# Optimization experiments

Measured on AMD Instinct MI355X. Metric: run time of the kernel, lower is better.

## Reference

```python
import jax, jax.numpy as jnp
import numpy as np

N_ATOMS = 4096
N_NEIGH = 32
IN_F = 128
HID = 256
OUT_F = 128
N_SPECIES = 64


def setup_inputs() -> dict:
    key = jax.random.key(0)
    k1, k2, k3, k4, k5, k6 = jax.random.split(key, 6)
    # kaiming-uniform-ish init scales (exact init doesn't matter for correctness testing)
    s1 = 1.0 / np.sqrt(IN_F)
    s2 = 1.0 / np.sqrt(HID)
    return {
        "features": jax.random.normal(k1, (N_ATOMS, N_NEIGH, IN_F), dtype=jnp.float32),
        "species_idx": jax.random.randint(k2, (N_ATOMS,), 0, N_SPECIES, dtype=jnp.int64 if jax.config.jax_enable_x64 else jnp.int32),
        "W1": jax.random.uniform(k3, (N_SPECIES, HID, IN_F), jnp.float32, -s1, s1),
        "b1": jax.random.uniform(k4, (N_SPECIES, HID), jnp.float32, -s1, s1),
        "W2": jax.random.uniform(k5, (N_SPECIES, OUT_F, HID), jnp.float32, -s2, s2),
        "b2": jax.random.uniform(k6, (N_SPECIES, OUT_F), jnp.float32, -s2, s2),
    }


def reference(features, species_idx, W1, b1, W2, b2):
    # Per-atom species-conditioned 2-layer MLP with SiLU after the hidden layer.
    # features: (A, N, in); W[idx]: (A, out, in) gathered per atom (as in torch W[idx]).
    x = jnp.einsum("ani,ahi->anh", features, W1[species_idx]) + b1[species_idx][:, None, :]
    x = jax.nn.silu(x)
    x = jnp.einsum("anh,aoh->ano", x, W2[species_idx]) + b2[species_idx][:, None, :]
    return x  # (A, N, out)
```

## Files before the change

kernel.cpp:

```cpp
#include <hip/hip_runtime.h>

typedef __attribute__((ext_vector_type(8))) short short8;
typedef __attribute__((ext_vector_type(4))) float f32x4;

#define N_ATOMS 4096
#define N_NEIGH 32
#define IN_F 128
#define HID 256
#define OUT_F 128
#define N_SPECIES 64
#define GRP 4
#define MAX_GROUPS 1088

struct HL { short h, l; };
__device__ __forceinline__ HL split2(float v) {
  unsigned u = __float_as_uint(v);
  float lo = v - __uint_as_float(u & 0xFFFF0000u);
  HL o;
  o.h = (short)(u >> 16);
  o.l = (short)(__float_as_uint(lo) >> 16);
  return o;
}

__global__ __launch_bounds__(256) void prep_kernel(
    const float* __restrict__ W1, const float* __restrict__ W2,
    const int* __restrict__ sp_idx,
    unsigned short* __restrict__ w1h, unsigned short* __restrict__ w1l,
    unsigned short* __restrict__ w2h, unsigned short* __restrict__ w2l,
    int* __restrict__ atom_order, int* __restrict__ grp_sp,
    int* __restrict__ grp_base, int* __restrict__ grp_cnt,
    int* __restrict__ n_groups) {
  const int t = threadIdx.x;
  if (blockIdx.x == 0) {
    __shared__ int cnt[N_SPECIES], off[N_SPECIES], cur[N_SPECIES], gb[N_SPECIES];
    if (t < N_SPECIES) cnt[t] = 0;
    __syncthreads();
    for (int a = t; a < N_ATOMS; a += 256) atomicAdd(&cnt[sp_idx[a]], 1);
    __syncthreads();
    if (t == 0) {
      int o = 0, g = 0;
      for (int s = 0; s < N_SPECIES; ++s) {
        off[s] = o; cur[s] = o; gb[s] = g;
        o += cnt[s];
        g += (cnt[s] + GRP - 1) / GRP;
      }
      *n_groups = g;
    }
    __syncthreads();
    for (int a = t; a < N_ATOMS; a += 256) {
      int s = sp_idx[a];
      atom_order[atomicAdd(&cur[s], 1)] = a;
    }
    if (t < N_SPECIES) {
      const int c = cnt[t], base = off[t], g0 = gb[t];
      const int ng = (c + GRP - 1) / GRP;
      for (int j = 0; j < ng; ++j) {
        grp_sp[g0 + j]   = t;
        grp_base[g0 + j] = base + j * GRP;
        grp_cnt[g0 + j]  = min(GRP, c - j * GRP);
      }
    }
    return;
  }
  const int NV = (N_SPECIES * HID * IN_F) / 4;
  const int nsplit = (gridDim.x - 1) * 256;
  for (int v = (blockIdx.x - 1) * 256 + t; v < 2 * NV; v += nsplit) {
    const float4* src; unsigned short* dh; unsigned short* dl; int j;
    if (v < NV) { src = (const float4*)W1; dh = w1h; dl = w1l; j = v; }
    else        { src = (const float4*)W2; dh = w2h; dl = w2l; j = v - NV; }
    float4 f = src[j];
    float vv[4] = {f.x, f.y, f.z, f.w};
    ushort4 h, l;
    HL s0 = split2(vv[0]); h.x = (unsigned short)s0.h; l.x = (unsigned short)s0.l;
    HL s1 = split2(vv[1]); h.y = (unsigned short)s1.h; l.y = (unsigned short)s1.l;
    HL s2 = split2(vv[2]); h.z = (unsigned short)s2.h; l.z = (unsigned short)s2.l;
    HL s3 = split2(vv[3]); h.w = (unsigned short)s3.h; l.w = (unsigned short)s3.l;
    ((ushort4*)dh)[j] = h;
    ((ushort4*)dl)[j] = l;
  }
}

__global__ __launch_bounds__(256, 2) void mlp_kernel(
    const float* __restrict__ feat,
    const float* __restrict__ b1g, const float* __restrict__ b2g,
    const unsigned short* __restrict__ w1h, const unsigned short* __restrict__ w1l,
    const unsigned short* __restrict__ w2h, const unsigned short* __restrict__ w2l,
    const int* __restrict__ atom_order, const int* __restrict__ grp_sp,
    const int* __restrict__ grp_base, const int* __restrict__ grp_cnt,
    const int* __restrict__ n_groups,
    float* __restrict__ out) {
  const int g = blockIdx.x;
  if (g >= *n_groups) return;
  const int s = grp_sp[g];
  const int abase = grp_base[g];
  const int cnt = grp_cnt[g];
  const int tid = threadIdx.x;
  const int wave = tid >> 6, lane = tid & 63;
  const int q = lane >> 4, r = lane & 15;

  __shared__ short8 lw1[2][2][512];
  __shared__ short8 lw2[2][2][512];
  __shared__ float lx[4][N_NEIGH * 32];

  const bool active = (wave < cnt);
  int atom = 0;

  int srcoff[8];
  const char* gplane;
  int hcstride;
  if (wave < 2) {
    gplane = (const char*)(wave == 0 ? w1h : w1l) + (long)s * (HID * IN_F) * 2;
    hcstride = 32 * IN_F * 2;
#pragma unroll
    for (int it = 0; it < 8; ++it) {
      const int d = it * 64 + lane;
      const int ks = d >> 7, ht = (d >> 6) & 1, rr = (d >> 2) & 15, qq = d & 3;
      srcoff[it] = (16 * ht + rr) * (IN_F * 2) + (32 * ks + 8 * qq) * 2;
    }
  } else {
    gplane = (const char*)(wave == 2 ? w2h : w2l) + (long)s * (OUT_F * HID) * 2;
    hcstride = 32 * 2;
#pragma unroll
    for (int it = 0; it < 8; ++it) {
      const int d = it * 64 + lane;
      const int ot = d >> 6, rr = (d >> 2) & 15, qq = d & 3;
      srcoff[it] = (16 * ot + rr) * (HID * 2) + qq * 16;
    }
  }
  short8* dst0 = (wave < 2) ? &lw1[0][wave][0] : &lw2[0][wave - 2][0];

  auto STAGE = [&](int buf, int hc) {
    const char* base = gplane + hc * hcstride;
    short8* dst = dst0 + buf * 1024;
#pragma unroll
    for (int it = 0; it < 8; ++it) {
      __builtin_amdgcn_global_load_lds(
          (const __attribute__((address_space(1))) unsigned int*)(base + srcoff[it]),
          (__attribute__((address_space(3))) unsigned int*)(dst + it * 64 + lane),
          16, 0, 0);
    }
  };

  STAGE(0, 0);

  short8 fh[2][4], fl[2][4];
  if (active) {
    atom = atom_order[abase + wave];
    const float* fb = feat + (long)atom * (N_NEIGH * IN_F);
#pragma unroll
    for (int nt = 0; nt < 2; ++nt)
#pragma unroll
      for (int ks = 0; ks < 4; ++ks) {
        const float* p = fb + (16 * nt + r) * IN_F + 32 * ks + 8 * q;
        float4 v0 = *(const float4*)p;
        float4 v1 = *(const float4*)(p + 4);
        float vv[8] = {v0.x, v0.y, v0.z, v0.w, v1.x, v1.y, v1.z, v1.w};
        short8 h8, l8;
#pragma unroll
        for (int j = 0; j < 8; ++j) {
          HL hl = split2(vv[j]);
          h8[j] = hl.h;
          l8[j] = hl.l;
        }
        fh[nt][ks] = h8;
        fl[nt][ks] = l8;
      }
  }

  float b2v[8];
#pragma unroll
  for (int ot = 0; ot < 8; ++ot) b2v[ot] = b2g[s * OUT_F + 16 * ot + r];

  f32x4 oacc[2][8] = {};
  char* lxw = (char*)lx[wave];
  const int slotbase = r * 4 + q;

  asm volatile("s_waitcnt vmcnt(0)" ::: "memory");
  __syncthreads();

  for (int hc = 0; hc < 8; ++hc) {
    const int buf = hc & 1;
    if (hc < 7) STAGE(buf ^ 1, hc + 1);

    if (active) {
      f32x4 xacc[2][2] = {};
#pragma unroll
      for (int ks = 0; ks < 4; ++ks)
#pragma unroll
        for (int ht = 0; ht < 2; ++ht) {
          short8 bh = lw1[buf][0][(ks * 2 + ht) * 64 + slotbase];
          short8 bl = lw1[buf][1][(ks * 2 + ht) * 64 + slotbase];
#pragma unroll
          for (int nt = 0; nt < 2; ++nt) {
            xacc[nt][ht] = __builtin_amdgcn_mfma_f32_16x16x32_bf16(fh[nt][ks], bh, xacc[nt][ht], 0, 0, 0);
            xacc[nt][ht] = __builtin_amdgcn_mfma_f32_16x16x32_bf16(fh[nt][ks], bl, xacc[nt][ht], 0, 0, 0);
            xacc[nt][ht] = __builtin_amdgcn_mfma_f32_16x16x32_bf16(fl[nt][ks], bh, xacc[nt][ht], 0, 0, 0);
          }
        }
#pragma unroll
      for (int ht = 0; ht < 2; ++ht) {
        const float b1v = b1g[s * HID + hc * 32 + 16 * ht + r];
#pragma unroll
        for (int nt = 0; nt < 2; ++nt)
#pragma unroll
          for (int i = 0; i < 4; ++i) {
            const int n = 16 * nt + 4 * q + i;
            float v = xacc[nt][ht][i] + b1v;
            v = v * __builtin_amdgcn_rcpf(1.0f + __expf(-v));
            int byte = (n << 7) + ((r + 16 * ht) << 2);
            byte ^= (n & 7) << 4;
            *(float*)(lxw + byte) = v;
          }
      }
      short8 ah[2], al[2];
#pragma unroll
      for (int nt = 0; nt < 2; ++nt) {
        const int n = 16 * nt + r;
        const int base_b = (n << 7) + (q << 5);
        const int swz = (n & 7) << 4;
        float4 v0 = *(const float4*)(lxw + (base_b ^ swz));
        float4 v1 = *(const float4*)(lxw + ((base_b + 16) ^ swz));
        float vv[8] = {v0.x, v0.y, v0.z, v0.w, v1.x, v1.y, v1.z, v1.w};
        short8 h8, l8;
#pragma unroll
        for (int j = 0; j < 8; ++j) {
          HL hl = split2(vv[j]);
          h8[j] = hl.h;
          l8[j] = hl.l;
        }
        ah[nt] = h8;
        al[nt] = l8;
      }
#pragma unroll
      for (int ot = 0; ot < 8; ++ot) {
        short8 bh = lw2[buf][0][ot * 64 + slotbase];
        short8 bl = lw2[buf][1][ot * 64 + slotbase];
#pragma unroll
        for (int nt = 0; nt < 2; ++nt) {
          oacc[nt][ot] = __builtin_amdgcn_mfma_f32_16x16x32_bf16(ah[nt], bh, oacc[nt][ot], 0, 0, 0);
          oacc[nt][ot] = __builtin_amdgcn_mfma_f32_16x16x32_bf16(ah[nt], bl, oacc[nt][ot], 0, 0, 0);
          oacc[nt][ot] = __builtin_amdgcn_mfma_f32_16x16x32_bf16(al[nt], bh, oacc[nt][ot], 0, 0, 0);
        }
      }
    }
    asm volatile("s_waitcnt vmcnt(0)" ::: "memory");
    __syncthreads();
  }

  if (active) {
    float* ob = out + (long)atom * (N_NEIGH * OUT_F);
#pragma unroll
    for (int nt = 0; nt < 2; ++nt)
#pragma unroll
      for (int ot = 0; ot < 8; ++ot)
#pragma unroll
        for (int i = 0; i < 4; ++i) {
          ob[(16 * nt + 4 * q + i) * OUT_F + 16 * ot + r] = oacc[nt][ot][i] + b2v[ot];
        }
  }
}

extern "C" void kernel_launch(void* const* d_in, const int* in_sizes, int n_in,
                              void* d_out, int out_size, void* d_ws, size_t ws_size,
                              hipStream_t stream) {
  const float* feat = (const float*)d_in[0];
  const int* sp     = (const int*)d_in[1];
  const float* W1   = (const float*)d_in[2];
  const float* b1   = (const float*)d_in[3];
  const float* W2   = (const float*)d_in[4];
  const float* b2   = (const float*)d_in[5];
  float* out = (float*)d_out;

  char* ws = (char*)d_ws;
  unsigned short* w1h = (unsigned short*)(ws + 0);
  unsigned short* w1l = (unsigned short*)(ws + 4194304);
  unsigned short* w2h = (unsigned short*)(ws + 8388608);
  unsigned short* w2l = (unsigned short*)(ws + 12582912);
  int* atom_order = (int*)(ws + 16777216);
  int* grp_sp     = (int*)(ws + 16777216 + 16384);
  int* grp_base   = (int*)(ws + 16777216 + 16384 + 4352);
  int* grp_cnt    = (int*)(ws + 16777216 + 16384 + 8704);
  int* n_groups   = (int*)(ws + 16777216 + 16384 + 13056);

  hipLaunchKernelGGL(prep_kernel, dim3(1025), dim3(256), 0, stream,
                     W1, W2, sp, w1h, w1l, w2h, w2l,
                     atom_order, grp_sp, grp_base, grp_cnt, n_groups);
  hipLaunchKernelGGL(mlp_kernel, dim3(MAX_GROUPS), dim3(256), 0, stream,
                     feat, b1, b2, w1h, w1l, w2h, w2l,
                     atom_order, grp_sp, grp_base, grp_cnt, n_groups, out);
}
```

Before: 203.0 us.

## Group eight atoms per block and stage swizzled weight tiles in LDS

Raises the number of atoms sharing a species group per block from four to eight, using 512-thread blocks, so each staged weight chunk serves twice as many waves. Weight staging now copies row-contiguous tiles with an XOR swizzle instead of the pre-permuted MFMA slot layout, with matching swizzled LDS reads to avoid bank conflicts. Block indices are also remapped to interleave groups across the grid. The trade-off is more idle waves in blocks whose species group has fewer than eight atoms, and higher per-block LDS and register pressure.

```diff
diff --git a/kernel.cpp b/kernel.cpp
--- a/kernel.cpp
+++ b/kernel.cpp
@@ -9,8 +9,8 @@
 #define HID 256
 #define OUT_F 128
 #define N_SPECIES 64
-#define GRP 4
-#define MAX_GROUPS 1088
+#define GRP 8
+#define MAX_GROUPS 576
 
 struct HL { short h, l; };
 __device__ __forceinline__ HL split2(float v) {
@@ -80,7 +80,7 @@
   }
 }
 
-__global__ __launch_bounds__(256, 2) void mlp_kernel(
+__global__ __launch_bounds__(512, 2) void mlp_kernel(
     const float* __restrict__ feat,
     const float* __restrict__ b1g, const float* __restrict__ b2g,
     const unsigned short* __restrict__ w1h, const unsigned short* __restrict__ w1l,
@@ -89,7 +89,8 @@
     const int* __restrict__ grp_base, const int* __restrict__ grp_cnt,
     const int* __restrict__ n_groups,
     float* __restrict__ out) {
-  const int g = blockIdx.x;
+  const int bid = blockIdx.x;
+  const int g = (bid & 7) * (MAX_GROUPS / 8) + (bid >> 3);
   if (g >= *n_groups) return;
   const int s = grp_sp[g];
   const int abase = grp_base[g];
@@ -98,45 +99,42 @@
   const int wave = tid >> 6, lane = tid & 63;
   const int q = lane >> 4, r = lane & 15;
 
-  __shared__ short8 lw1[2][2][512];
-  __shared__ short8 lw2[2][2][512];
-  __shared__ float lx[4][N_NEIGH * 32];
+  __shared__ short lw1[2][2][32 * IN_F];
+  __shared__ short lw2[2][2][OUT_F * 32];
+  __shared__ float lx[8][N_NEIGH * 32];
 
   const bool active = (wave < cnt);
   int atom = 0;
 
-  int srcoff[8];
-  const char* gplane;
-  int hcstride;
-  if (wave < 2) {
-    gplane = (const char*)(wave == 0 ? w1h : w1l) + (long)s * (HID * IN_F) * 2;
-    hcstride = 32 * IN_F * 2;
-#pragma unroll
-    for (int it = 0; it < 8; ++it) {
-      const int d = it * 64 + lane;
-      const int ks = d >> 7, ht = (d >> 6) & 1, rr = (d >> 2) & 15, qq = d & 3;
-      srcoff[it] = (16 * ht + rr) * (IN_F * 2) + (32 * ks + 8 * qq) * 2;
-    }
-  } else {
-    gplane = (const char*)(wave == 2 ? w2h : w2l) + (long)s * (OUT_F * HID) * 2;
-    hcstride = 32 * 2;
-#pragma unroll
-    for (int it = 0; it < 8; ++it) {
-      const int d = it * 64 + lane;
-      const int ot = d >> 6, rr = (d >> 2) & 15, qq = d & 3;
-      srcoff[it] = (16 * ot + rr) * (HID * 2) + qq * 16;
-    }
-  }
-  short8* dst0 = (wave < 2) ? &lw1[0][wave][0] : &lw2[0][wave - 2][0];
+  const int plane = wave >> 1, half = wave & 1;
+  const bool isw1 = (plane < 2);
+  const unsigned short* pl = (plane == 0) ? w1h : (plane == 1) ? w1l
+                           : (plane == 2) ? w2h : w2l;
+  const char* gplane = (const char*)pl + (long)s * (HID * IN_F) * 2;
+  const int hcstride = isw1 ? (32 * IN_F * 2) : (32 * 2);
+  int srcoff[4], dstoff[4];
+#pragma unroll
+  for (int it = 0; it < 4; ++it) {
+    const int b = half * 4096 + it * 1024 + lane * 16;
+    if (isw1) {
+      const int row = b >> 8;
+      srcoff[it] = row * (IN_F * 2) + ((b & 255) ^ ((row & 7) << 4));
+    } else {
+      const int o = b >> 6;
+      srcoff[it] = o * (HID * 2) + ((b & 63) ^ (((o >> 1) & 3) << 4));
+    }
+    dstoff[it] = b;
+  }
+  char* lplane0 = isw1 ? (char*)lw1[0][plane] : (char*)lw2[0][plane - 2];
 
   auto STAGE = [&](int buf, int hc) {
     const char* base = gplane + hc * hcstride;
-    short8* dst = dst0 + buf * 1024;
-#pragma unroll
-    for (int it = 0; it < 8; ++it) {
+    char* lp = lplane0 + buf * 16384;
+#pragma unroll
+    for (int it = 0; it < 4; ++it) {
       __builtin_amdgcn_global_load_lds(
           (const __attribute__((address_space(1))) unsigned int*)(base + srcoff[it]),
-          (__attribute__((address_space(3))) unsigned int*)(dst + it * 64 + lane),
+          (__attribute__((address_space(3))) unsigned int*)(lp + dstoff[it]),
           16, 0, 0);
     }
   };
@@ -173,7 +171,8 @@
 
   f32x4 oacc[2][8] = {};
   char* lxw = (char*)lx[wave];
-  const int slotbase = r * 4 + q;
+  const int swz1 = (r & 7) << 4;
+  const int swz2 = ((r >> 1) & 3) << 4;
 
   asm volatile("s_waitcnt vmcnt(0)" ::: "memory");
   __syncthreads();
@@ -184,12 +183,16 @@
 
     if (active) {
       f32x4 xacc[2][2] = {};
-#pragma unroll
-      for (int ks = 0; ks < 4; ++ks)
+      const char* L1h = (const char*)lw1[buf][0];
+      const char* L1l = (const char*)lw1[buf][1];
+#pragma unroll
+      for (int ks = 0; ks < 4; ++ks) {
+        const int koff = 64 * ks + 16 * q;
 #pragma unroll
         for (int ht = 0; ht < 2; ++ht) {
-          short8 bh = lw1[buf][0][(ks * 2 + ht) * 64 + slotbase];
-          short8 bl = lw1[buf][1][(ks * 2 + ht) * 64 + slotbase];
+          const int byte = (16 * ht + r) * 256 + (koff ^ swz1);
+          short8 bh = *(const short8*)(L1h + byte);
+          short8 bl = *(const short8*)(L1l + byte);
 #pragma unroll
           for (int nt = 0; nt < 2; ++nt) {
             xacc[nt][ht] = __builtin_amdgcn_mfma_f32_16x16x32_bf16(fh[nt][ks], bh, xacc[nt][ht], 0, 0, 0);
@@ -197,6 +200,7 @@
             xacc[nt][ht] = __builtin_amdgcn_mfma_f32_16x16x32_bf16(fl[nt][ks], bh, xacc[nt][ht], 0, 0, 0);
           }
         }
+      }
 #pragma unroll
       for (int ht = 0; ht < 2; ++ht) {
         const float b1v = b1g[s * HID + hc * 32 + 16 * ht + r];
@@ -231,10 +235,13 @@
         ah[nt] = h8;
         al[nt] = l8;
       }
+      const char* L2h = (const char*)lw2[buf][0];
+      const char* L2l = (const char*)lw2[buf][1];
 #pragma unroll
       for (int ot = 0; ot < 8; ++ot) {
-        short8 bh = lw2[buf][0][ot * 64 + slotbase];
-        short8 bl = lw2[buf][1][ot * 64 + slotbase];
+        const int byte = (16 * ot + r) * 64 + ((16 * q) ^ swz2);
+        short8 bh = *(const short8*)(L2h + byte);
+        short8 bl = *(const short8*)(L2l + byte);
 #pragma unroll
         for (int nt = 0; nt < 2; ++nt) {
           oacc[nt][ot] = __builtin_amdgcn_mfma_f32_16x16x32_bf16(ah[nt], bh, oacc[nt][ot], 0, 0, 0);
@@ -285,7 +292,7 @@
   hipLaunchKernelGGL(prep_kernel, dim3(1025), dim3(256), 0, stream,
                      W1, W2, sp, w1h, w1l, w2h, w2l,
                      atom_order, grp_sp, grp_base, grp_cnt, n_groups);
-  hipLaunchKernelGGL(mlp_kernel, dim3(MAX_GROUPS), dim3(256), 0, stream,
+  hipLaunchKernelGGL(mlp_kernel, dim3(MAX_GROUPS), dim3(512), 0, stream,
                      feat, b1, b2, w1h, w1l, w2h, w2l,
                      atom_order, grp_sp, grp_base, grp_cnt, n_groups, out);
 }
```

New measurement: 205.7 us. About the same (+1.4%).
